# Performance work log

Measured on AMD Instinct MI355X. Metric: run time of the kernel, lower is better.

The kernel has to match this reference:

```python
import jax, jax.numpy as jnp
import numpy as np

B, C, H, W = 8, 256, 96, 96
NQ, NCLS = 100, 12
OBJ_CH = NCLS - 2 + 1  # 11
EPS = 1e-6


def conv2d(x, w, b, pad):
    out = jax.lax.conv_general_dilated(x, w, (1, 1), [(pad, pad), (pad, pad)],
                                       dimension_numbers=('NCHW', 'OIHW', 'NCHW'))
    return out + b[None, :, None, None]


def conv1d(x, w, b):
    out = jax.lax.conv_general_dilated(x, w, (1,), [(0, 0)],
                                       dimension_numbers=('NCH', 'OIH', 'NCH'))
    return out + b[None, :, None]


def adaptive_avg_pool_1d(x, out_size):
    # x: [..., L]; torch AdaptiveAvgPool semantics: bin i = mean(x[floor(i*L/o):ceil((i+1)*L/o)])
    L = x.shape[-1]
    i = np.arange(out_size)
    starts = (i * L) // out_size
    ends = -((-(i + 1) * L) // out_size)
    csum = jnp.concatenate([jnp.zeros(x.shape[:-1] + (1,), x.dtype), jnp.cumsum(x, -1)], -1)
    sizes = jnp.asarray((ends - starts).astype(np.float32))
    return (csum[..., ends] - csum[..., starts]) / sizes


def local_max(p):
    # 8-neighbor local maximum with zero padding, thresholded at EPS
    pd = jnp.pad(p, ((0, 0), (0, 0), (1, 1), (1, 1)))
    m = ((p >= pd[:, :, :-2, 1:-1]) & (p >= pd[:, :, 2:, 1:-1]) &
         (p >= pd[:, :, 1:-1, :-2]) & (p >= pd[:, :, 1:-1, 2:]) &
         (p >= pd[:, :, :-2, :-2]) & (p >= pd[:, :, :-2, 2:]) &
         (p >= pd[:, :, 2:, :-2]) & (p >= pd[:, :, 2:, 2:]) & (p >= EPS))
    return m.astype(p.dtype)


def mask_and_nms(probs):
    # one-hot mask from argmax over foreground channels, then add local-max map
    oh = jax.nn.one_hot(jnp.argmax(probs[:, :-1], axis=1), probs.shape[1], axis=1, dtype=probs.dtype)
    p = probs * oh
    return p + local_max(p)


def head(x, w1, b1, w2, b2):
    return conv2d(jax.nn.relu(conv2d(x, w1, b1, 1)), w2, b2, 0)


def setup_inputs() -> dict:
    key = jax.random.key(0)
    ks = jax.random.split(key, 20)
    rn = lambda k, s: jax.random.normal(k, s, jnp.float32) * 0.02
    z = lambda n: jnp.zeros((n,), jnp.float32)
    return {
        'x': jax.random.normal(ks[0], (B, C, H, W), jnp.float32),
        'y': jax.random.normal(ks[1], (B, C, H, W), jnp.float32),
        'pos_embeddings': jax.random.normal(ks[2], (1, C, H, W), jnp.float32),
        'lw1': rn(ks[3], (C, C, 3, 3)), 'lb1': z(C),
        'lw2': rn(ks[4], (2, C, 1, 1)), 'lb2': z(2),
        'rw1': rn(ks[5], (C, C, 3, 3)), 'rb1': z(C),
        'rw2': rn(ks[6], (2, C, 1, 1)), 'rb2': z(2),
        'ow1': rn(ks[7], (C, C, 3, 3)), 'ob1': z(C),
        'ow2': rn(ks[8], (OBJ_CH, C, 1, 1)), 'ob2': z(OBJ_CH),
        'cw1': rn(ks[9], (64, C, 3, 3)), 'cb1': z(64),
        'cw2': rn(ks[10], (32, 64, 3, 3)), 'cb2': z(32),
        'cm_lw': rn(ks[11], (778 * 2, 778 * 32)), 'cm_lb': z(778 * 2),
        'c1d_w': rn(ks[12], (C, 2, 3)), 'c1d_b': z(C),
        'q_lw': rn(ks[13], (NQ * C, C)), 'q_lb': z(NQ * C),
    }


def reference(x, y, pos_embeddings, lw1, lb1, lw2, lb2, rw1, rb1, rw2, rb2,
              ow1, ob1, ow2, ob2, cw1, cb1, cw2, cb2, cm_lw, cm_lb,
              c1d_w, c1d_b, q_lw, q_lb):
    b = x.shape[0]
    left_logits = head(x, lw1, lb1, lw2, lb2)
    right_logits = head(x, rw1, rb1, rw2, rb2)
    obj_logits = head(x, ow1, ob1, ow2, ob2)

    left_p = mask_and_nms(jax.nn.softmax(left_logits, axis=1))
    right_p = mask_and_nms(jax.nn.softmax(right_logits, axis=1))
    obj_p = mask_and_nms(jax.nn.softmax(obj_logits, axis=1))

    hw = H * W
    idx_l = jax.lax.top_k(left_p[:, 0].reshape(b, hw), 40)[1]
    idx_r = jax.lax.top_k(right_p[:, 0].reshape(b, hw), 40)[1]
    idx_o = jax.lax.top_k(obj_p[:, :-1].reshape(b, OBJ_CH - 1, hw).max(axis=1), 20)[1]
    idx = jnp.concatenate([idx_l, idx_r, idx_o], axis=1)  # [B, 100]

    xf = x.reshape(b, C, hw)
    topk_proposals = jnp.take_along_axis(xf, jnp.broadcast_to(idx[:, None, :], (b, C, NQ)), axis=2)
    pf = jnp.broadcast_to(pos_embeddings, (b, C, H, W)).reshape(b, C, hw)
    topk_pos = jnp.take_along_axis(pf, jnp.broadcast_to(idx[:, None, :], (b, C, NQ)), axis=2)

    # contact map estimation branch
    h = jax.nn.relu(conv2d(y, cw1, cb1, 1))
    h = jax.nn.relu(conv2d(h, cw2, cb2, 1))  # [B,32,H,W]
    h = jnp.mean(h, axis=3)                  # adaptive pool width -> 1
    h = adaptive_avg_pool_1d(h, 778)         # [B,32,778]
    cm = h.reshape(b, -1) @ cm_lw.T + cm_lb  # [B,1556]
    contact_map = cm.reshape(b, 2, 778, 1)

    # ContactMapConvolution
    cc = conv1d(contact_map.reshape(b, 2, 778), c1d_w, c1d_b)  # [B,C,776]
    cc = jnp.mean(cc, axis=2)                                  # [B,C]
    feat = (cc @ q_lw.T + q_lb).reshape(b, C, NQ)              # [B,C,100]

    topk_proposals = topk_proposals + feat
    return (topk_proposals, topk_pos, left_logits, right_logits, obj_logits, contact_map)
```

## Files before the change

### kernel.cpp

```cpp
#include <hip/hip_runtime.h>
#include <float.h>
#include <math.h>

#define B_ 8
#define C_ 256
#define H_ 96
#define W_ 96
#define HW_ 9216
#define TOTPIX_ 73728
#define NQ_ 100
#define EPS_ 1e-6f

typedef unsigned short ushort_t;
typedef __attribute__((ext_vector_type(8))) short bf16x8;
typedef __attribute__((ext_vector_type(4))) float f32x4;

typedef __attribute__((address_space(3))) unsigned int as3_u32;
typedef __attribute__((address_space(1))) unsigned int as1_u32;

__device__ __forceinline__ void gl16(const void* g, void* l) {
    __builtin_amdgcn_global_load_lds(
        (const as1_u32*)(unsigned long long)g,
        (as3_u32*)(unsigned int)(unsigned long long)l, 16, 0, 0);
}

__device__ __forceinline__ ushort_t bf16_of(float v) {
    unsigned u = __float_as_uint(v);
    u += 0x7fffu + ((u >> 16) & 1u);
    return (ushort_t)(u >> 16);
}
__device__ __forceinline__ float f_of_bf16(ushort_t h) {
    return __uint_as_float((unsigned)h << 16);
}

__global__ __launch_bounds__(256)
void tsplit_kernel(const float* __restrict__ in, ushort_t* __restrict__ oh,
                   ushort_t* __restrict__ ol)
{
    __shared__ float T[32][33];
    const int tx = threadIdx.x & 31, ty = threadIdx.x >> 5;
    const int p0 = blockIdx.x * 32, ci0 = blockIdx.y * 32, b = blockIdx.z;
#pragma unroll
    for (int i = 0; i < 4; ++i)
        T[ty + 8*i][tx] = in[((size_t)b*C_ + ci0 + ty + 8*i)*HW_ + p0 + tx];
    __syncthreads();
#pragma unroll
    for (int i = 0; i < 4; ++i) {
        float v = T[tx][ty + 8*i];
        ushort_t hi = bf16_of(v);
        float lo = v - f_of_bf16(hi);
        size_t o = ((size_t)b*HW_ + p0 + ty + 8*i)*C_ + ci0 + tx;
        oh[o] = hi;
        ol[o] = bf16_of(lo);
    }
}

__global__ __launch_bounds__(256)
void repack_kernel(const float* __restrict__ w, ushort_t* __restrict__ wh,
                   ushort_t* __restrict__ wl, int Cout, int Cin)
{
    int id = blockIdx.x*256 + threadIdx.x;
    int tot = 9*Cout*Cin;
    if (id >= tot) return;
    int tap = id / (Cout*Cin);
    int r = id - tap*(Cout*Cin);
    int oc = r / Cin, ci = r - oc*Cin;
    float v = w[((size_t)oc*Cin + ci)*9 + tap];
    ushort_t hi = bf16_of(v);
    wh[id] = hi;
    wl[id] = bf16_of(v - f_of_bf16(hi));
}

template<int WM, int WN, int MF, int NF, int CIN, int MODE, int KK>
__global__ __launch_bounds__(WM*WN*64, 4)
void conv_gemm_kernel(const ushort_t* __restrict__ Agh, const ushort_t* __restrict__ Agl,
                      const ushort_t* __restrict__ Wgh, const ushort_t* __restrict__ Wgl,
                      const float* __restrict__ bias1,
                      const float* __restrict__ w2, const float* __restrict__ b2,
                      float* __restrict__ out_logits,
                      ushort_t* __restrict__ Oth, ushort_t* __restrict__ Otl,
                      float* __restrict__ outf)
{
    constexpr int NW   = WM*WN;
    constexpr int NT   = NW*64;
    constexpr int BM   = WM*MF*16;
    constexpr int COUT = WN*NF*16;
    constexpr int APAD = ((BM + 194 + 7) / 8) * 8;
    constexpr int NCALL_A = (2*APAD*4)/64;
    constexpr int NCALL_B = (2*COUT*4)/64;

    __shared__ __align__(16) ushort_t ALds[2*APAD*32];
    __shared__ __align__(16) ushort_t BLds[2*COUT*32];

    const int tid  = threadIdx.x;
    const int lane = tid & 63;
    const int wid  = __builtin_amdgcn_readfirstlane(tid >> 6);
    const int wm   = wid / WN, wn = wid % WN;
    const int l15  = lane & 15, l4 = lane >> 4;
    const int wmb  = wm * MF * 16;
    const int wnb  = wn * NF * 16;

    const int p0    = blockIdx.x * BM;
    const int bidx  = p0 / HW_;
    const int pimg0 = p0 - bidx * HW_;

    int vmask[MF];
#pragma unroll
    for (int mf = 0; mf < MF; ++mf) {
        int q  = pimg0 + wmb + mf*16 + l15;
        int yy = q / 96, xx = q - yy*96;
        int m = 0;
#pragma unroll
        for (int t = 0; t < 9; ++t) {
            int dy = t/3, dx = t - dy*3;
            if ((unsigned)(yy+dy-1) < 96u && (unsigned)(xx+dx-1) < 96u) m |= 1<<t;
        }
        vmask[mf] = m;
    }

    f32x4 acc[MF][NF];
#pragma unroll
    for (int i = 0; i < MF; ++i)
#pragma unroll
        for (int j = 0; j < NF; ++j) acc[i][j] = (f32x4){0.f,0.f,0.f,0.f};

#pragma unroll 1
    for (int ci0 = 0; ci0 < CIN; ci0 += 32) {
#pragma unroll 1
        for (int c = wid; c < NCALL_A; c += NW) {
            int id    = c*64 + lane;
            int split = id / (APAD*4);
            int r     = id - split*(APAD*4);
            int pix   = r >> 2, kg = r & 3;
            long P = (long)p0 - 97 + pix;
            P = P < 0 ? 0 : (P > (TOTPIX_-1) ? (TOTPIX_-1) : P);
            const ushort_t* src = (split ? Agl : Agh)
                + (size_t)P*CIN + ci0 + ((kg ^ (pix & 3)) << 3);
            gl16(src, ALds + (size_t)c*512);
        }
#pragma unroll 1
        for (int tap = 0; tap < 9; ++tap) {
#pragma unroll 1
            for (int c = wid; c < NCALL_B; c += NW) {
                int id    = c*64 + lane;
                int split = id / (COUT*4);
                int r     = id - split*(COUT*4);
                int n     = r >> 2, kg = r & 3;
                const ushort_t* src = (split ? Wgl : Wgh)
                    + ((size_t)tap*COUT + n)*CIN + ci0 + kg*8;
                gl16(src, BLds + (size_t)c*512);
            }
            __syncthreads();

            const int dy = tap/3, dx = tap - dy*3;
            const int offt = (dy-1)*96 + (dx-1);

            bf16x8 bh[NF], bl[NF];
#pragma unroll
            for (int nf = 0; nf < NF; ++nf) {
                int bi = (wnb + nf*16 + l15)*32 + l4*8;
                bh[nf] = *(const bf16x8*)&BLds[bi];
                bl[nf] = *(const bf16x8*)&BLds[bi + COUT*32];
            }
#pragma unroll
            for (int mf = 0; mf < MF; ++mf) {
                int row = wmb + mf*16 + l15 + 97 + offt;
                int ai  = row*32 + ((l4 ^ (row & 3)) << 3);
                bf16x8 ah = *(const bf16x8*)&ALds[ai];
                bf16x8 al = *(const bf16x8*)&ALds[ai + APAD*32];
                bool ok = (vmask[mf] >> tap) & 1;
                bf16x8 z = (bf16x8)(short)0;
                ah = ok ? ah : z;
                al = ok ? al : z;
#pragma unroll
                for (int nf = 0; nf < NF; ++nf) {
                    acc[mf][nf] = __builtin_amdgcn_mfma_f32_16x16x32_bf16(
                        ah, bh[nf], acc[mf][nf], 0, 0, 0);
                    acc[mf][nf] = __builtin_amdgcn_mfma_f32_16x16x32_bf16(
                        al, bh[nf], acc[mf][nf], 0, 0, 0);
                    acc[mf][nf] = __builtin_amdgcn_mfma_f32_16x16x32_bf16(
                        ah, bl[nf], acc[mf][nf], 0, 0, 0);
                }
            }
            __syncthreads();
        }
    }

    float biasv[NF];
#pragma unroll
    for (int nf = 0; nf < NF; ++nf) biasv[nf] = bias1[wnb + nf*16 + l15];

    if constexpr (MODE == 0) {
        float* Lacc = (float*)BLds;
        float w2v[NF][KK];
#pragma unroll
        for (int nf = 0; nf < NF; ++nf)
#pragma unroll
            for (int k = 0; k < KK; ++k)
                w2v[nf][k] = w2[(size_t)k*COUT + wnb + nf*16 + l15];

#pragma unroll
        for (int mf = 0; mf < MF; ++mf) {
#pragma unroll
            for (int reg = 0; reg < 4; ++reg) {
                float v[KK];
#pragma unroll
                for (int k = 0; k < KK; ++k) v[k] = 0.f;
#pragma unroll
                for (int nf = 0; nf < NF; ++nf) {
                    float r = fmaxf(acc[mf][nf][reg] + biasv[nf], 0.f);
#pragma unroll
                    for (int k = 0; k < KK; ++k) v[k] += r * w2v[nf][k];
                }
#pragma unroll
                for (int k = 0; k < KK; ++k) {
                    v[k] += __shfl_xor(v[k], 1);
                    v[k] += __shfl_xor(v[k], 2);
                    v[k] += __shfl_xor(v[k], 4);
                    v[k] += __shfl_xor(v[k], 8);
                }
                if (l15 == 0) {
                    int mrow = wmb + mf*16 + l4*4 + reg;
#pragma unroll
                    for (int k = 0; k < KK; ++k)
                        Lacc[((size_t)wn*BM + mrow)*KK + k] = v[k];
                }
            }
        }
        __syncthreads();
        for (int i = tid; i < BM*KK; i += NT) {
            int mrow = i / KK, k = i - mrow*KK;
            float s = b2[k];
#pragma unroll
            for (int w = 0; w < WN; ++w) s += Lacc[((size_t)w*BM + mrow)*KK + k];
            out_logits[((size_t)bidx*KK + k)*HW_ + pimg0 + mrow] = s;
        }
    } else if constexpr (MODE == 1) {
#pragma unroll
        for (int mf = 0; mf < MF; ++mf)
#pragma unroll
            for (int nf = 0; nf < NF; ++nf)
#pragma unroll
                for (int reg = 0; reg < 4; ++reg) {
                    float r = fmaxf(acc[mf][nf][reg] + biasv[nf], 0.f);
                    ushort_t hi = bf16_of(r);
                    float lo = r - f_of_bf16(hi);
                    size_t P = (size_t)p0 + wmb + mf*16 + l4*4 + reg;
                    size_t o = P*COUT + wnb + nf*16 + l15;
                    Oth[o] = hi;
                    Otl[o] = bf16_of(lo);
                }
    } else {
#pragma unroll
        for (int mf = 0; mf < MF; ++mf)
#pragma unroll
            for (int nf = 0; nf < NF; ++nf)
#pragma unroll
                for (int reg = 0; reg < 4; ++reg) {
                    float r = fmaxf(acc[mf][nf][reg] + biasv[nf], 0.f);
                    int mrow = wmb + mf*16 + l4*4 + reg;
                    outf[((size_t)bidx*COUT + wnb + nf*16 + l15)*HW_ + pimg0 + mrow] = r;
                }
    }
}

__global__ __launch_bounds__(256)
void prob2_kernel(const float* __restrict__ logits, float* __restrict__ p0)
{
    int i = blockIdx.x * 256 + threadIdx.x;
    if (i >= B_ * HW_) return;
    int b = i / HW_, pix = i - b * HW_;
    float l0 = logits[(size_t)b * 2 * HW_ + pix];
    float l1 = logits[(size_t)b * 2 * HW_ + HW_ + pix];
    float m = fmaxf(l0, l1);
    float e0 = expf(l0 - m), e1 = expf(l1 - m);
    p0[i] = e0 / (e0 + e1);
}

__global__ __launch_bounds__(256)
void score2_kernel(const float* __restrict__ p, float* __restrict__ sc)
{
    int i = blockIdx.x * 256 + threadIdx.x;
    if (i >= B_ * HW_) return;
    int pix = i % HW_;
    int yy = pix / W_, xx = pix - (pix / W_) * W_;
    float c = p[i];
    bool ok = (c >= EPS_);
    const float* pb = p + (i - pix);
#pragma unroll
    for (int dy = -1; dy <= 1; ++dy)
#pragma unroll
        for (int dx = -1; dx <= 1; ++dx) {
            if (dy == 0 && dx == 0) continue;
            int ny = yy + dy, nx = xx + dx;
            float v = 0.f;
            if (ny >= 0 && ny < H_ && nx >= 0 && nx < W_) v = pb[ny * W_ + nx];
            ok = ok && (c >= v);
        }
    sc[i] = c + (ok ? 1.f : 0.f);
}

__global__ __launch_bounds__(256)
void probobj_kernel(const float* __restrict__ logits, float* __restrict__ pval,
                    int* __restrict__ cstar)
{
    int i = blockIdx.x * 256 + threadIdx.x;
    if (i >= B_ * HW_) return;
    int b = i / HW_, pix = i - b * HW_;
    const float* lb = logits + (size_t)b * 11 * HW_ + pix;
    float l[11];
#pragma unroll
    for (int c2 = 0; c2 < 11; ++c2) l[c2] = lb[(size_t)c2 * HW_];
    float m = l[0];
#pragma unroll
    for (int c2 = 1; c2 < 11; ++c2) m = fmaxf(m, l[c2]);
    float sum = 0.f;
#pragma unroll
    for (int c2 = 0; c2 < 11; ++c2) sum += expf(l[c2] - m);
    int a = 0; float bestl = l[0];
#pragma unroll
    for (int c2 = 1; c2 < 10; ++c2)
        if (l[c2] > bestl) { bestl = l[c2]; a = c2; }
    pval[i] = expf(bestl - m) / sum;
    cstar[i] = a;
}

__global__ __launch_bounds__(256)
void score11_kernel(const float* __restrict__ p, const int* __restrict__ cs,
                    float* __restrict__ sc)
{
    int i = blockIdx.x * 256 + threadIdx.x;
    if (i >= B_ * HW_) return;
    int pix = i % HW_;
    int yy = pix / W_, xx = pix - (pix / W_) * W_;
    float c = p[i];
    int cc = cs[i];
    bool ok = (c >= EPS_);
    int base = i - pix;
#pragma unroll
    for (int dy = -1; dy <= 1; ++dy)
#pragma unroll
        for (int dx = -1; dx <= 1; ++dx) {
            if (dy == 0 && dx == 0) continue;
            int ny = yy + dy, nx = xx + dx;
            float v = 0.f;
            if (ny >= 0 && ny < H_ && nx >= 0 && nx < W_) {
                int n = base + ny * W_ + nx;
                v = (cs[n] == cc) ? p[n] : 0.f;
            }
            ok = ok && (c >= v);
        }
    sc[i] = c + (ok ? 1.f : 0.f);
}

__global__ __launch_bounds__(256)
void topk_kernel(const float* __restrict__ scL, const float* __restrict__ scR,
                 const float* __restrict__ scO, int* __restrict__ idx)
{
    __shared__ float sv[HW_];
    __shared__ float rv[256];
    __shared__ int   ri[256];
    const int h = blockIdx.x, b = blockIdx.y;
    const float* src = (h == 0) ? scL : (h == 1) ? scR : scO;
    const int k = (h == 2) ? 20 : 40;
    const int off = b * NQ_ + ((h == 0) ? 0 : (h == 1) ? 40 : 80);

    for (int t = threadIdx.x; t < HW_; t += 256) sv[t] = src[(size_t)b * HW_ + t];
    __syncthreads();

    for (int kk = 0; kk < k; ++kk) {
        float bestv = -FLT_MAX; int besti = HW_;
        for (int t = threadIdx.x; t < HW_; t += 256) {
            float v = sv[t];
            if (v > bestv) { bestv = v; besti = t; }
        }
        rv[threadIdx.x] = bestv; ri[threadIdx.x] = besti;
        __syncthreads();
        for (int s = 128; s > 0; s >>= 1) {
            if (threadIdx.x < s) {
                float v2 = rv[threadIdx.x + s]; int i2 = ri[threadIdx.x + s];
                if (v2 > rv[threadIdx.x] ||
                    (v2 == rv[threadIdx.x] && i2 < ri[threadIdx.x])) {
                    rv[threadIdx.x] = v2; ri[threadIdx.x] = i2;
                }
            }
            __syncthreads();
        }
        if (threadIdx.x == 0) { idx[off + kk] = ri[0]; sv[ri[0]] = -FLT_MAX; }
        __syncthreads();
    }
}

__global__ __launch_bounds__(128)
void pool_kernel(const float* __restrict__ h2, float* __restrict__ pooled)
{
    int bc = blockIdx.x;
    __shared__ float row[96];
    for (int hh = threadIdx.x; hh < 96; hh += 128) {
        const float* p = h2 + (size_t)bc * HW_ + hh * W_;
        float s = 0.f;
        for (int ww = 0; ww < 96; ++ww) s += p[ww];
        row[hh] = s * (1.f / 96.f);
    }
    __syncthreads();
    for (int i = threadIdx.x; i < 778; i += 128) {
        int s0 = (i * 96) / 778;
        int e0 = ((i + 1) * 96 + 777) / 778;
        float s = 0.f;
        for (int t = s0; t < e0; ++t) s += row[t];
        pooled[(size_t)bc * 778 + i] = s / (float)(e0 - s0);
    }
}

__global__ __launch_bounds__(256)
void cm_kernel(const float* __restrict__ pooled, const float* __restrict__ cm_lw,
               const float* __restrict__ cm_lb, float* __restrict__ out5)
{
    const int j = blockIdx.x;
    const float* wr = cm_lw + (size_t)j * 24896;
    float acc[8];
#pragma unroll
    for (int b = 0; b < 8; ++b) acc[b] = 0.f;
    for (int t = threadIdx.x; t < 24896; t += 256) {
        float w = wr[t];
#pragma unroll
        for (int b = 0; b < 8; ++b) acc[b] += w * pooled[(size_t)b * 24896 + t];
    }
    __shared__ float red[8][256];
#pragma unroll
    for (int b = 0; b < 8; ++b) red[b][threadIdx.x] = acc[b];
    __syncthreads();
    for (int s = 128; s > 0; s >>= 1) {
        if (threadIdx.x < s) {
#pragma unroll
            for (int b = 0; b < 8; ++b) red[b][threadIdx.x] += red[b][threadIdx.x + s];
        }
        __syncthreads();
    }
    if (threadIdx.x < 8)
        out5[(size_t)threadIdx.x * 1556 + j] = red[threadIdx.x][0] + cm_lb[j];
}

__global__ __launch_bounds__(256)
void c1d_kernel(const float* __restrict__ cmap, const float* __restrict__ w,
                const float* __restrict__ bias, float* __restrict__ ccmean)
{
    int b = blockIdx.x;
    __shared__ float r[2][778];
    __shared__ float T[2][3];
    for (int t = threadIdx.x; t < 1556; t += 256)
        r[t / 778][t % 778] = cmap[(size_t)b * 1556 + t];
    __syncthreads();
    if (threadIdx.x < 2) {
        int ic = threadIdx.x;
        float s = 0.f;
        for (int i2 = 0; i2 < 778; ++i2) s += r[ic][i2];
        T[ic][0] = s - r[ic][776] - r[ic][777];
        T[ic][1] = s - r[ic][0]   - r[ic][777];
        T[ic][2] = s - r[ic][0]   - r[ic][1];
    }
    __syncthreads();
    int oc = threadIdx.x;
    float a = 0.f;
#pragma unroll
    for (int ic = 0; ic < 2; ++ic)
#pragma unroll
        for (int k = 0; k < 3; ++k)
            a += w[oc * 6 + ic * 3 + k] * T[ic][k];
    ccmean[b * 256 + oc] = a / 776.f + bias[oc];
}

__global__ __launch_bounds__(256)
void feat_kernel(const float* __restrict__ ccmean, const float* __restrict__ q_lw,
                 const float* __restrict__ q_lb, float* __restrict__ feat)
{
    __shared__ float cc[8][256];
    for (int t = threadIdx.x; t < 2048; t += 256) cc[t >> 8][t & 255] = ccmean[t];
    __syncthreads();
    int j = blockIdx.x * 256 + threadIdx.x;
    const float* wr = q_lw + (size_t)j * 256;
    float acc[8];
#pragma unroll
    for (int b = 0; b < 8; ++b) acc[b] = 0.f;
    for (int c = 0; c < 256; ++c) {
        float wv = wr[c];
#pragma unroll
        for (int b = 0; b < 8; ++b) acc[b] += wv * cc[b][c];
    }
    float qb = q_lb[j];
#pragma unroll
    for (int b = 0; b < 8; ++b) feat[(size_t)b * 25600 + j] = acc[b] + qb;
}

__global__ __launch_bounds__(256)
void gather_kernel(const float* __restrict__ x, const float* __restrict__ pos,
                   const float* __restrict__ feat, const int* __restrict__ idx,
                   float* __restrict__ out0, float* __restrict__ out1)
{
    int t = blockIdx.x * 256 + threadIdx.x;
    if (t >= B_ * C_ * NQ_) return;
    int q = t % NQ_;
    int c2 = (t / NQ_) % C_;
    int b = t / (C_ * NQ_);
    int p = idx[b * NQ_ + q];
    out0[t] = x[((size_t)b * C_ + c2) * HW_ + p] + feat[(size_t)b * 25600 + c2 * NQ_ + q];
    out1[t] = pos[(size_t)c2 * HW_ + p];
}

extern "C" void kernel_launch(void* const* d_in, const int* in_sizes, int n_in,
                              void* d_out, int out_size, void* d_ws, size_t ws_size,
                              hipStream_t stream) {
    const float* x    = (const float*)d_in[0];
    const float* y    = (const float*)d_in[1];
    const float* pos  = (const float*)d_in[2];
    const float* lw1  = (const float*)d_in[3];  const float* lb1 = (const float*)d_in[4];
    const float* lw2  = (const float*)d_in[5];  const float* lb2 = (const float*)d_in[6];
    const float* rw1  = (const float*)d_in[7];  const float* rb1 = (const float*)d_in[8];
    const float* rw2  = (const float*)d_in[9];  const float* rb2 = (const float*)d_in[10];
    const float* ow1  = (const float*)d_in[11]; const float* ob1 = (const float*)d_in[12];
    const float* ow2  = (const float*)d_in[13]; const float* ob2 = (const float*)d_in[14];
    const float* cw1  = (const float*)d_in[15]; const float* cb1 = (const float*)d_in[16];
    const float* cw2  = (const float*)d_in[17]; const float* cb2 = (const float*)d_in[18];
    const float* cmlw = (const float*)d_in[19]; const float* cmlb = (const float*)d_in[20];
    const float* c1dw = (const float*)d_in[21]; const float* c1db = (const float*)d_in[22];
    const float* qlw  = (const float*)d_in[23]; const float* qlb  = (const float*)d_in[24];

    float* out  = (float*)d_out;
    float* out0 = out;
    float* out1 = out + 204800;
    float* out2 = out + 409600;
    float* out3 = out + 557056;
    float* out4 = out + 704512;
    float* out5 = out + 1515520;

    float* ws = (float*)d_ws;
    ushort_t* Rh   = (ushort_t*)(ws);
    ushort_t* Rl   = (ushort_t*)(ws + 9437184);
    ushort_t* h1h  = (ushort_t*)(ws + 18874368);
    ushort_t* h1l  = (ushort_t*)(ws + 21233664);
    float*    h2   = ws + 23592960;
    ushort_t* wLh  = (ushort_t*)(ws + 25952256);
    ushort_t* wLl  = (ushort_t*)(ws + 26247168);
    ushort_t* wRh  = (ushort_t*)(ws + 26542080);
    ushort_t* wRl  = (ushort_t*)(ws + 26836992);
    ushort_t* wOh  = (ushort_t*)(ws + 27131904);
    ushort_t* wOl  = (ushort_t*)(ws + 27426816);
    ushort_t* wc1h = (ushort_t*)(ws + 27721728);
    ushort_t* wc1l = (ushort_t*)(ws + 27795456);
    ushort_t* wc2h = (ushort_t*)(ws + 27869184);
    ushort_t* wc2l = (ushort_t*)(ws + 27878400);
    float* pooled  = ws + 27887616;
    float* ccmean  = ws + 28086784;
    float* feat    = ws + 28088832;
    float* pmap    = ws + 28293632;
    int*   csmap   = (int*)(ws + 28367360);
    float* scL     = ws + 28441088;
    float* scR     = ws + 28514816;
    float* scO     = ws + 28588544;
    int*   idxb    = (int*)(ws + 28662272);
    (void)in_sizes; (void)n_in; (void)out_size; (void)ws_size; (void)pos;

    repack_kernel<<<(9*256*256+255)/256, 256, 0, stream>>>(lw1, wLh, wLl, 256, 256);
    repack_kernel<<<(9*256*256+255)/256, 256, 0, stream>>>(rw1, wRh, wRl, 256, 256);
    repack_kernel<<<(9*256*256+255)/256, 256, 0, stream>>>(ow1, wOh, wOl, 256, 256);
    repack_kernel<<<(9*64*256+255)/256,  256, 0, stream>>>(cw1, wc1h, wc1l, 64, 256);
    repack_kernel<<<(9*32*64+255)/256,   256, 0, stream>>>(cw2, wc2h, wc2l, 32, 64);

    tsplit_kernel<<<dim3(288, 8, 8), 256, 0, stream>>>(y, Rh, Rl);
    conv_gemm_kernel<4,2,2,2,256,1,1><<<576, 512, 0, stream>>>(
        Rh, Rl, wc1h, wc1l, cb1, nullptr, nullptr, nullptr, h1h, h1l, nullptr);
    conv_gemm_kernel<4,2,2,1,64,2,1><<<576, 512, 0, stream>>>(
        h1h, h1l, wc2h, wc2l, cb2, nullptr, nullptr, nullptr, nullptr, nullptr, h2);
    pool_kernel<<<256, 128, 0, stream>>>(h2, pooled);
    cm_kernel<<<1556, 256, 0, stream>>>(pooled, cmlw, cmlb, out5);
    c1d_kernel<<<8, 256, 0, stream>>>(out5, c1dw, c1db, ccmean);
    feat_kernel<<<100, 256, 0, stream>>>(ccmean, qlw, qlb, feat);

    tsplit_kernel<<<dim3(288, 8, 8), 256, 0, stream>>>(x, Rh, Rl);
    conv_gemm_kernel<2,4,4,4,256,0,2><<<576, 512, 0, stream>>>(
        Rh, Rl, wLh, wLl, lb1, lw2, lb2, out2, nullptr, nullptr, nullptr);
    conv_gemm_kernel<2,4,4,4,256,0,2><<<576, 512, 0, stream>>>(
        Rh, Rl, wRh, wRl, rb1, rw2, rb2, out3, nullptr, nullptr, nullptr);
    conv_gemm_kernel<2,4,4,4,256,0,11><<<576, 512, 0, stream>>>(
        Rh, Rl, wOh, wOl, ob1, ow2, ob2, out4, nullptr, nullptr, nullptr);

    prob2_kernel<<<288, 256, 0, stream>>>(out2, pmap);
    score2_kernel<<<288, 256, 0, stream>>>(pmap, scL);
    prob2_kernel<<<288, 256, 0, stream>>>(out3, pmap);
    score2_kernel<<<288, 256, 0, stream>>>(pmap, scR);
    probobj_kernel<<<288, 256, 0, stream>>>(out4, pmap, csmap);
    score11_kernel<<<288, 256, 0, stream>>>(pmap, csmap, scO);

    topk_kernel<<<dim3(3, 8), 256, 0, stream>>>(scL, scR, scO, idxb);
    gather_kernel<<<800, 256, 0, stream>>>(x, pos, feat, idxb, out0, out1);
}
```

Before: 1.406 ms.

## Switch conv GEMM to 32x32 MFMA with double-buffered LDS staging

The implicit-GEMM conv kernel now uses 32x32x16 bf16 MFMA tiles instead of 16x16x32, and steps over K in chunks of 16 channels. A and B tiles are double-buffered in LDS so the next tap or channel group loads while the current one computes, with one barrier per step instead of two. Blocks are remapped across the grid for locality, and the fp32-output mode transposes through LDS so global writes are coalesced. This adds more barriers per K (smaller chunks) and larger accumulators per thread, which may affect occupancy.

```diff
diff --git a/kernel.cpp b/kernel.cpp
--- a/kernel.cpp
+++ b/kernel.cpp
@@ -13,7 +13,7 @@
 
 typedef unsigned short ushort_t;
 typedef __attribute__((ext_vector_type(8))) short bf16x8;
-typedef __attribute__((ext_vector_type(4))) float f32x4;
+typedef __attribute__((ext_vector_type(16))) float f32x16;
 
 typedef __attribute__((address_space(3))) unsigned int as3_u32;
 typedef __attribute__((address_space(1))) unsigned int as1_u32;
@@ -71,7 +71,7 @@
     wl[id] = bf16_of(v - f_of_bf16(hi));
 }
 
-template<int WM, int WN, int MF, int NF, int CIN, int MODE, int KK>
+template<int WM, int WN, int MFR, int NFR, int CIN, int MODE, int KK>
 __global__ __launch_bounds__(WM*WN*64, 4)
 void conv_gemm_kernel(const ushort_t* __restrict__ Agh, const ushort_t* __restrict__ Agl,
                       const ushort_t* __restrict__ Wgh, const ushort_t* __restrict__ Wgl,
@@ -81,33 +81,40 @@
                       ushort_t* __restrict__ Oth, ushort_t* __restrict__ Otl,
                       float* __restrict__ outf)
 {
-    constexpr int NW   = WM*WN;
-    constexpr int NT   = NW*64;
-    constexpr int BM   = WM*MF*16;
-    constexpr int COUT = WN*NF*16;
-    constexpr int APAD = ((BM + 194 + 7) / 8) * 8;
-    constexpr int NCALL_A = (2*APAD*4)/64;
-    constexpr int NCALL_B = (2*COUT*4)/64;
-
-    __shared__ __align__(16) ushort_t ALds[2*APAD*32];
-    __shared__ __align__(16) ushort_t BLds[2*COUT*32];
+    constexpr int NW    = WM*WN;
+    constexpr int NT    = NW*64;
+    constexpr int BM    = WM*MFR*32;
+    constexpr int COUT  = WN*NFR*32;
+    constexpr int NG    = CIN/16;
+    constexpr int NSTEP = NG*9;
+    constexpr int APAD  = ((BM + 194 + 15)/16)*16;
+    constexpr int ASZ   = 2*APAD*16;
+    constexpr int BSZ   = 2*COUT*16;
+    constexpr int ACALLS = APAD/16;
+    constexpr int BCALLS = COUT/16;
+
+    __shared__ __align__(16) ushort_t ALds[2*ASZ];
+    __shared__ __align__(16) ushort_t BLds[2*BSZ];
 
     const int tid  = threadIdx.x;
     const int lane = tid & 63;
     const int wid  = __builtin_amdgcn_readfirstlane(tid >> 6);
     const int wm   = wid / WN, wn = wid % WN;
-    const int l15  = lane & 15, l4 = lane >> 4;
-    const int wmb  = wm * MF * 16;
-    const int wnb  = wn * NF * 16;
-
-    const int p0    = blockIdx.x * BM;
+    const int l31  = lane & 31, hh2 = lane >> 5;
+    const int wmb  = wm * MFR * 32;
+    const int wnb  = wn * NFR * 32;
+
+    const int cpx = gridDim.x >> 3;
+    const int bid = (blockIdx.x & 7)*cpx + (blockIdx.x >> 3);
+
+    const int p0    = bid * BM;
     const int bidx  = p0 / HW_;
     const int pimg0 = p0 - bidx * HW_;
 
-    int vmask[MF];
-#pragma unroll
-    for (int mf = 0; mf < MF; ++mf) {
-        int q  = pimg0 + wmb + mf*16 + l15;
+    int vmask[MFR];
+#pragma unroll
+    for (int mf = 0; mf < MFR; ++mf) {
+        int q  = pimg0 + wmb + mf*32 + l31;
         int yy = q / 96, xx = q - yy*96;
         int m = 0;
 #pragma unroll
@@ -118,99 +125,125 @@
         vmask[mf] = m;
     }
 
-    f32x4 acc[MF][NF];
-#pragma unroll
-    for (int i = 0; i < MF; ++i)
-#pragma unroll
-        for (int j = 0; j < NF; ++j) acc[i][j] = (f32x4){0.f,0.f,0.f,0.f};
-
+    auto stageA = [&](int g, int sel) {
+        ushort_t* dst = ALds + sel*ASZ;
+        int ci0 = g*16;
 #pragma unroll 1
-    for (int ci0 = 0; ci0 < CIN; ci0 += 32) {
+        for (int c = wid; c < ACALLS; c += NW) {
+            int id    = c*64 + lane;
+            int split = id / (2*APAD);
+            int r2    = id - split*2*APAD;
+            int pix   = r2 >> 1, ch = r2 & 1;
+            int P = p0 - 97 + pix;
+            P = P < 0 ? 0 : (P > (TOTPIX_-1) ? (TOTPIX_-1) : P);
+            int ch2 = ch ^ (pix & 1);
+            const ushort_t* src = (split ? Agl : Agh)
+                + (size_t)P*CIN + ci0 + ch2*8;
+            gl16(src, dst + (size_t)c*512);
+        }
+    };
+    auto stageB = [&](int g, int tap, int sel) {
+        ushort_t* dst = BLds + sel*BSZ;
+        int ci0 = g*16;
 #pragma unroll 1
-        for (int c = wid; c < NCALL_A; c += NW) {
+        for (int c = wid; c < BCALLS; c += NW) {
             int id    = c*64 + lane;
-            int split = id / (APAD*4);
-            int r     = id - split*(APAD*4);
-            int pix   = r >> 2, kg = r & 3;
-            long P = (long)p0 - 97 + pix;
-            P = P < 0 ? 0 : (P > (TOTPIX_-1) ? (TOTPIX_-1) : P);
-            const ushort_t* src = (split ? Agl : Agh)
-                + (size_t)P*CIN + ci0 + ((kg ^ (pix & 3)) << 3);
-            gl16(src, ALds + (size_t)c*512);
-        }
+            int split = id / (2*COUT);
+            int r2    = id - split*2*COUT;
+            int row   = r2 >> 1, ch = r2 & 1;
+            int ch2 = ch ^ (row & 1);
+            const ushort_t* src = (split ? Wgl : Wgh)
+                + ((size_t)tap*COUT + row)*CIN + ci0 + ch2*8;
+            gl16(src, dst + (size_t)c*512);
+        }
+    };
+
+    f32x16 acc[MFR][NFR];
+#pragma unroll
+    for (int i = 0; i < MFR; ++i)
+#pragma unroll
+        for (int j = 0; j < NFR; ++j)
+#pragma unroll
+            for (int r = 0; r < 16; ++r) acc[i][j][r] = 0.f;
+
+    stageA(0, 0);
+    stageB(0, 0, 0);
+    __syncthreads();
+
+    int g = 0, tap = 0;
 #pragma unroll 1
-        for (int tap = 0; tap < 9; ++tap) {
-#pragma unroll 1
-            for (int c = wid; c < NCALL_B; c += NW) {
-                int id    = c*64 + lane;
-                int split = id / (COUT*4);
-                int r     = id - split*(COUT*4);
-                int n     = r >> 2, kg = r & 3;
-                const ushort_t* src = (split ? Wgl : Wgh)
-                    + ((size_t)tap*COUT + n)*CIN + ci0 + kg*8;
-                gl16(src, BLds + (size_t)c*512);
+    for (int step = 0; step < NSTEP; ++step) {
+        if (tap == 0 && g + 1 < NG) stageA(g + 1, (g + 1) & 1);
+        if (step + 1 < NSTEP) {
+            int nt = tap + 1, ng = g;
+            if (nt == 9) { nt = 0; ng = g + 1; }
+            stageB(ng, nt, (step + 1) & 1);
+        }
+
+        const int abase = (g & 1) * ASZ;
+        const int bbase = (step & 1) * BSZ;
+        const int offt  = (tap/3)*96 + (tap - (tap/3)*3) - 97;
+
+        bf16x8 bh[NFR], bl[NFR];
+#pragma unroll
+        for (int nf = 0; nf < NFR; ++nf) {
+            int n  = wnb + nf*32 + l31;
+            int ch = hh2 ^ (n & 1);
+            int o  = bbase + n*16 + ch*8;
+            bh[nf] = *(const bf16x8*)&BLds[o];
+            bl[nf] = *(const bf16x8*)&BLds[o + COUT*16];
+        }
+#pragma unroll
+        for (int mf = 0; mf < MFR; ++mf) {
+            int row = 97 + offt + wmb + mf*32 + l31;
+            int ch  = hh2 ^ (row & 1);
+            int o   = abase + row*16 + ch*8;
+            bf16x8 ah = *(const bf16x8*)&ALds[o];
+            bf16x8 al = *(const bf16x8*)&ALds[o + APAD*16];
+            bool ok = (vmask[mf] >> tap) & 1;
+            bf16x8 z = (bf16x8)(short)0;
+            ah = ok ? ah : z;
+            al = ok ? al : z;
+#pragma unroll
+            for (int nf = 0; nf < NFR; ++nf) {
+                acc[mf][nf] = __builtin_amdgcn_mfma_f32_32x32x16_bf16(
+                    ah, bh[nf], acc[mf][nf], 0, 0, 0);
+                acc[mf][nf] = __builtin_amdgcn_mfma_f32_32x32x16_bf16(
+                    al, bh[nf], acc[mf][nf], 0, 0, 0);
+                acc[mf][nf] = __builtin_amdgcn_mfma_f32_32x32x16_bf16(
+                    ah, bl[nf], acc[mf][nf], 0, 0, 0);
             }
-            __syncthreads();
-
-            const int dy = tap/3, dx = tap - dy*3;
-            const int offt = (dy-1)*96 + (dx-1);
-
-            bf16x8 bh[NF], bl[NF];
-#pragma unroll
-            for (int nf = 0; nf < NF; ++nf) {
-                int bi = (wnb + nf*16 + l15)*32 + l4*8;
-                bh[nf] = *(const bf16x8*)&BLds[bi];
-                bl[nf] = *(const bf16x8*)&BLds[bi + COUT*32];
-            }
-#pragma unroll
-            for (int mf = 0; mf < MF; ++mf) {
-                int row = wmb + mf*16 + l15 + 97 + offt;
-                int ai  = row*32 + ((l4 ^ (row & 3)) << 3);
-                bf16x8 ah = *(const bf16x8*)&ALds[ai];
-                bf16x8 al = *(const bf16x8*)&ALds[ai + APAD*32];
-                bool ok = (vmask[mf] >> tap) & 1;
-                bf16x8 z = (bf16x8)(short)0;
-                ah = ok ? ah : z;
-                al = ok ? al : z;
-#pragma unroll
-                for (int nf = 0; nf < NF; ++nf) {
-                    acc[mf][nf] = __builtin_amdgcn_mfma_f32_16x16x32_bf16(
-                        ah, bh[nf], acc[mf][nf], 0, 0, 0);
-                    acc[mf][nf] = __builtin_amdgcn_mfma_f32_16x16x32_bf16(
-                        al, bh[nf], acc[mf][nf], 0, 0, 0);
-                    acc[mf][nf] = __builtin_amdgcn_mfma_f32_16x16x32_bf16(
-                        ah, bl[nf], acc[mf][nf], 0, 0, 0);
-                }
-            }
-            __syncthreads();
-        }
-    }
-
-    float biasv[NF];
-#pragma unroll
-    for (int nf = 0; nf < NF; ++nf) biasv[nf] = bias1[wnb + nf*16 + l15];
+        }
+        __syncthreads();
+
+        if (++tap == 9) { tap = 0; ++g; }
+    }
+
+    float biasv[NFR];
+#pragma unroll
+    for (int nf = 0; nf < NFR; ++nf) biasv[nf] = bias1[wnb + nf*32 + l31];
 
     if constexpr (MODE == 0) {
         float* Lacc = (float*)BLds;
-        float w2v[NF][KK];
-#pragma unroll
-        for (int nf = 0; nf < NF; ++nf)
+        float w2v[NFR][KK];
+#pragma unroll
+        for (int nf = 0; nf < NFR; ++nf)
 #pragma unroll
             for (int k = 0; k < KK; ++k)
-                w2v[nf][k] = w2[(size_t)k*COUT + wnb + nf*16 + l15];
-
-#pragma unroll
-        for (int mf = 0; mf < MF; ++mf) {
-#pragma unroll
-            for (int reg = 0; reg < 4; ++reg) {
+                w2v[nf][k] = w2[(size_t)k*COUT + wnb + nf*32 + l31];
+
+#pragma unroll
+        for (int mf = 0; mf < MFR; ++mf) {
+#pragma unroll
+            for (int r = 0; r < 16; ++r) {
                 float v[KK];
 #pragma unroll
                 for (int k = 0; k < KK; ++k) v[k] = 0.f;
 #pragma unroll
-                for (int nf = 0; nf < NF; ++nf) {
-                    float r = fmaxf(acc[mf][nf][reg] + biasv[nf], 0.f);
-#pragma unroll
-                    for (int k = 0; k < KK; ++k) v[k] += r * w2v[nf][k];
+                for (int nf = 0; nf < NFR; ++nf) {
+                    float rr = fmaxf(acc[mf][nf][r] + biasv[nf], 0.f);
+#pragma unroll
+                    for (int k = 0; k < KK; ++k) v[k] += rr * w2v[nf][k];
                 }
 #pragma unroll
                 for (int k = 0; k < KK; ++k) {
@@ -218,9 +251,10 @@
                     v[k] += __shfl_xor(v[k], 2);
                     v[k] += __shfl_xor(v[k], 4);
                     v[k] += __shfl_xor(v[k], 8);
+                    v[k] += __shfl_xor(v[k], 16);
                 }
-                if (l15 == 0) {
-                    int mrow = wmb + mf*16 + l4*4 + reg;
+                if (l31 == 0) {
+                    int mrow = wmb + mf*32 + (r & 3) + 8*(r >> 2) + 4*hh2;
 #pragma unroll
                     for (int k = 0; k < KK; ++k)
                         Lacc[((size_t)wn*BM + mrow)*KK + k] = v[k];
@@ -237,30 +271,35 @@
         }
     } else if constexpr (MODE == 1) {
 #pragma unroll
-        for (int mf = 0; mf < MF; ++mf)
-#pragma unroll
-            for (int nf = 0; nf < NF; ++nf)
-#pragma unroll
-                for (int reg = 0; reg < 4; ++reg) {
-                    float r = fmaxf(acc[mf][nf][reg] + biasv[nf], 0.f);
-                    ushort_t hi = bf16_of(r);
-                    float lo = r - f_of_bf16(hi);
-                    size_t P = (size_t)p0 + wmb + mf*16 + l4*4 + reg;
-                    size_t o = P*COUT + wnb + nf*16 + l15;
+        for (int mf = 0; mf < MFR; ++mf)
+#pragma unroll
+            for (int nf = 0; nf < NFR; ++nf)
+#pragma unroll
+                for (int r = 0; r < 16; ++r) {
+                    float rr = fmaxf(acc[mf][nf][r] + biasv[nf], 0.f);
+                    ushort_t hi = bf16_of(rr);
+                    float lo = rr - f_of_bf16(hi);
+                    int mrow = (r & 3) + 8*(r >> 2) + 4*hh2;
+                    size_t P = (size_t)p0 + wmb + mf*32 + mrow;
+                    size_t o = P*COUT + wnb + nf*32 + l31;
                     Oth[o] = hi;
                     Otl[o] = bf16_of(lo);
                 }
     } else {
-#pragma unroll
-        for (int mf = 0; mf < MF; ++mf)
-#pragma unroll
-            for (int nf = 0; nf < NF; ++nf)
-#pragma unroll
-                for (int reg = 0; reg < 4; ++reg) {
-                    float r = fmaxf(acc[mf][nf][reg] + biasv[nf], 0.f);
-                    int mrow = wmb + mf*16 + l4*4 + reg;
-                    outf[((size_t)bidx*COUT + wnb + nf*16 + l15)*HW_ + pimg0 + mrow] = r;
-                }
+        float (*T)[257] = (float(*)[257])ALds;
+#pragma unroll
+        for (int mf = 0; mf < MFR; ++mf)
+#pragma unroll
+            for (int r = 0; r < 16; ++r) {
+                float rr = fmaxf(acc[mf][0][r] + biasv[0], 0.f);
+                int mrow = wmb + mf*32 + (r & 3) + 8*(r >> 2) + 4*hh2;
+                T[l31][mrow] = rr;
+            }
+        __syncthreads();
+        for (int i = tid; i < COUT*BM; i += NT) {
+            int c = i / BM, m = i - c*BM;
+            outf[((size_t)bidx*COUT + c)*HW_ + pimg0 + m] = T[c][m];
+        }
     }
 }
 
@@ -567,9 +606,9 @@
     repack_kernel<<<(9*32*64+255)/256,   256, 0, stream>>>(cw2, wc2h, wc2l, 32, 64);
 
     tsplit_kernel<<<dim3(288, 8, 8), 256, 0, stream>>>(y, Rh, Rl);
-    conv_gemm_kernel<4,2,2,2,256,1,1><<<576, 512, 0, stream>>>(
+    conv_gemm_kernel<4,2,1,1,256,1,1><<<576, 512, 0, stream>>>(
         Rh, Rl, wc1h, wc1l, cb1, nullptr, nullptr, nullptr, h1h, h1l, nullptr);
-    conv_gemm_kernel<4,2,2,1,64,2,1><<<576, 512, 0, stream>>>(
+    conv_gemm_kernel<8,1,1,1,64,2,1><<<288, 512, 0, stream>>>(
         h1h, h1l, wc2h, wc2l, cb2, nullptr, nullptr, nullptr, nullptr, nullptr, h2);
     pool_kernel<<<256, 128, 0, stream>>>(h2, pooled);
     cm_kernel<<<1556, 256, 0, stream>>>(pooled, cmlw, cmlb, out5);
@@ -577,11 +616,11 @@
     feat_kernel<<<100, 256, 0, stream>>>(ccmean, qlw, qlb, feat);
 
     tsplit_kernel<<<dim3(288, 8, 8), 256, 0, stream>>>(x, Rh, Rl);
-    conv_gemm_kernel<2,4,4,4,256,0,2><<<576, 512, 0, stream>>>(
+    conv_gemm_kernel<2,4,2,2,256,0,2><<<576, 512, 0, stream>>>(
         Rh, Rl, wLh, wLl, lb1, lw2, lb2, out2, nullptr, nullptr, nullptr);
-    conv_gemm_kernel<2,4,4,4,256,0,2><<<576, 512, 0, stream>>>(
+    conv_gemm_kernel<2,4,2,2,256,0,2><<<576, 512, 0, stream>>>(
         Rh, Rl, wRh, wRl, rb1, rw2, rb2, out3, nullptr, nullptr, nullptr);
-    conv_gemm_kernel<2,4,4,4,256,0,11><<<576, 512, 0, stream>>>(
+    conv_gemm_kernel<2,4,2,2,256,0,11><<<576, 512, 0, stream>>>(
         Rh, Rl, wOh, wOl, ob1, ow2, ob2, out4, nullptr, nullptr, nullptr);
 
     prob2_kernel<<<288, 256, 0, stream>>>(out2, pmap);
```

New measurement: 1.584 ms. 1.13x slower.
